# Kernel optimization log

Measured on AMD Instinct MI355X. Metric: run time of the kernel, lower is better.

Reference implementation:

```python
import jax, jax.numpy as jnp
import numpy as np

B, N, T_FULL, T, KS, FEAT = 32, 360, 512, 64, 8, 8
NLAYERS = 3   # DCGRU layers
GLAYERS = 4   # bidirectional GRU layers in GruKRegion


def _gru_layer(x, Wih, Whh, bih, bhh, reverse):
    # x: [M, Tg, in] -> [M, Tg, H]; PyTorch GRU gate order (r, z, n)
    M = x.shape[0]
    Hh = Whh.shape[1]
    xp = jnp.einsum('mti,gi->mtg', x, Wih) + bih  # precompute input projections
    if reverse:
        xp = xp[:, ::-1]

    def step(h, xg):
        gh = jnp.einsum('mh,gh->mg', h, Whh) + bhh
        xr, xz, xn = jnp.split(xg, 3, -1)
        hr, hz, hn = jnp.split(gh, 3, -1)
        r = jax.nn.sigmoid(xr + hr)
        z = jax.nn.sigmoid(xz + hz)
        n = jnp.tanh(xn + r * hn)
        hnew = (1.0 - z) * n + z * h
        return hnew, hnew

    _, hs = jax.lax.scan(step, jnp.zeros((M, Hh), x.dtype), jnp.swapaxes(xp, 0, 1))
    hs = jnp.swapaxes(hs, 0, 1)
    if reverse:
        hs = hs[:, ::-1]
    return hs


def _dcgru_cell(x, h, adj, gw, gb, cw, cb):
    # x, h: [B, N] (rnn_units = 1); adj: [B, N, N]; max_diffusion_step = 2
    def gconv(inp, st, W, bias):
        x0 = jnp.stack([inp, st], axis=-1)                     # [B,N,2]
        x1 = jnp.einsum('bnm,bmc->bnc', adj, x0)
        x2 = 2.0 * jnp.einsum('bnm,bmc->bnc', adj, x1) - x0    # Chebyshev recurrence
        # torch layout: [B,N,C,num_matrices] flattened channel-major
        xc = jnp.stack([x0, x1, x2], axis=-1).reshape(x0.shape[0], N, 6)
        return jnp.einsum('bnf,fo->bno', xc, W) + bias

    gates = jax.nn.sigmoid(gconv(x, h, gw, gb))                # [B,N,2]
    r, u = gates[..., 0], gates[..., 1]
    c = jnp.tanh(gconv(x, r * h, cw, cb)[..., 0])
    return u * h + (1.0 - u) * c


def _forward(full_seq, reconstruct_seq, node_feas, temperature,
             g0wih, g0whh, g0bih, g0bhh, gwih, gwhh, gbih, gbhh,
             l1w, l1b, l2w, l2b,
             enc_gw, enc_gb, enc_cw, enc_cb,
             dec_gw, dec_gb, dec_cw, dec_cb, proj_w, proj_b):
    b, n, tfull = full_seq.shape
    # ---- GruKRegion feature extractor ----
    x = full_seq.reshape(b * n, tfull // KS, KS)
    out = jnp.concatenate(
        [_gru_layer(x, g0wih[0], g0whh[0], g0bih[0], g0bhh[0], False),
         _gru_layer(x, g0wih[1], g0whh[1], g0bih[1], g0bhh[1], True)], axis=-1)
    for l in range(GLAYERS - 1):
        out = jnp.concatenate(
            [_gru_layer(out, gwih[l, 0], gwhh[l, 0], gbih[l, 0], gbhh[l, 0], False),
             _gru_layer(out, gwih[l, 1], gwhh[l, 1], gbih[l, 1], gbhh[l, 1], True)], axis=-1)
    feat = out[:, -1, :].reshape(b, n, 2 * KS)
    feat = jax.nn.leaky_relu(jnp.einsum('bnf,of->bno', feat, l1w) + l1b, 0.2)
    feat = jnp.einsum('bnf,of->bno', feat, l2w) + l2b          # [B,N,FEAT]
    # ---- Embed2GraphByProduct ----
    logits = jnp.einsum('bjk,bpk->bjp', feat, feat)            # [B,N,N]
    # ---- hard gumbel softmax ----
    U = jax.random.uniform(jax.random.key(42), logits.shape, logits.dtype)
    g = -jnp.log(-jnp.log(U + 1e-10) + 1e-10)
    y_soft = jax.nn.softmax((logits + g) / temperature, axis=-1)
    y_hard = jax.nn.one_hot(jnp.argmax(y_soft, -1), n, dtype=y_soft.dtype)
    adj = y_soft + jax.lax.stop_gradient(y_hard - y_soft)
    adj = jnp.where(jnp.eye(n, dtype=bool), 0.0, adj)          # zero diagonal
    # (original computes a random-walk matrix then discards it; skipped)
    # ---- encoder: scan over time, 3 stacked DCGRU layers ----
    seq = jnp.transpose(reconstruct_seq, (2, 0, 1))            # [T,B,N]

    def enc_step(hid, xt):
        o = xt
        new = []
        for l in range(NLAYERS):
            hnew = _dcgru_cell(o, hid[l], adj, enc_gw[l], enc_gb[l], enc_cw[l], enc_cb[l])
            new.append(hnew)
            o = hnew
        return jnp.stack(new), None

    hid, _ = jax.lax.scan(enc_step, jnp.zeros((NLAYERS, b, n), seq.dtype), seq)

    def dec_step(carry, _):
        hidc, inp = carry
        o = inp
        new = []
        for l in range(NLAYERS):
            hnew = _dcgru_cell(o, hidc[l], adj, dec_gw[l], dec_gb[l], dec_cw[l], dec_cb[l])
            new.append(hnew)
            o = hnew
        proj = o * proj_w[0, 0] + proj_b[0]                    # Linear(1,1)
        return (jnp.stack(new), proj), proj

    _, outs = jax.lax.scan(dec_step, (hid, jnp.zeros((b, n), seq.dtype)), None, length=T)
    return jnp.transpose(outs, (1, 2, 0))                      # [B,N,T]


def setup_inputs():
    key = jax.random.key(0)
    ks = jax.random.split(key, 24)
    s = 0.2
    p = lambda k, sh: jax.random.normal(k, sh, jnp.float32) * s
    return dict(
        full_seq=jax.random.normal(ks[0], (B, N, T_FULL), jnp.float32),
        reconstruct_seq=jax.random.normal(ks[1], (B, N, T), jnp.float32),
        node_feas=jax.random.normal(ks[2], (B, N, KS), jnp.float32),
        temperature=jnp.ones((), jnp.float32),
        g0wih=p(ks[3], (2, 3 * KS, KS)), g0whh=p(ks[4], (2, 3 * KS, KS)),
        g0bih=p(ks[5], (2, 3 * KS)), g0bhh=p(ks[6], (2, 3 * KS)),
        gwih=p(ks[7], (GLAYERS - 1, 2, 3 * KS, 2 * KS)),
        gwhh=p(ks[8], (GLAYERS - 1, 2, 3 * KS, KS)),
        gbih=p(ks[9], (GLAYERS - 1, 2, 3 * KS)), gbhh=p(ks[10], (GLAYERS - 1, 2, 3 * KS)),
        l1w=p(ks[11], (KS, 2 * KS)), l1b=p(ks[12], (KS,)),
        l2w=p(ks[13], (FEAT, KS)), l2b=p(ks[14], (FEAT,)),
        enc_gw=p(ks[15], (NLAYERS, 6, 2)), enc_gb=jnp.ones((NLAYERS, 2), jnp.float32),
        enc_cw=p(ks[16], (NLAYERS, 6, 1)), enc_cb=jnp.zeros((NLAYERS, 1), jnp.float32),
        dec_gw=p(ks[17], (NLAYERS, 6, 2)), dec_gb=jnp.ones((NLAYERS, 2), jnp.float32),
        dec_cw=p(ks[18], (NLAYERS, 6, 1)), dec_cb=jnp.zeros((NLAYERS, 1), jnp.float32),
        proj_w=p(ks[19], (1, 1)), proj_b=jnp.zeros((1,), jnp.float32),
    )


def reference(full_seq, reconstruct_seq, node_feas, temperature,
              g0wih, g0whh, g0bih, g0bhh, gwih, gwhh, gbih, gbhh,
              l1w, l1b, l2w, l2b,
              enc_gw, enc_gb, enc_cw, enc_cb,
              dec_gw, dec_gb, dec_cw, dec_cb, proj_w, proj_b):
    return _forward(full_seq, reconstruct_seq, node_feas, temperature,
                    g0wih, g0whh, g0bih, g0bhh, gwih, gwhh, gbih, gbhh,
                    l1w, l1b, l2w, l2b,
                    enc_gw, enc_gb, enc_cw, enc_cb,
                    dec_gw, dec_gb, dec_cw, dec_cb, proj_w, proj_b)
```

## Files before the change

kernel.cpp:

```cpp
#include <hip/hip_runtime.h>
#include <math.h>

#define M_SEQ 11520
#define NNODE 360
#define NB    32
#define TT    64

__device__ __forceinline__ float fsigd(float x)  { return 1.0f / (1.0f + __expf(-x)); }
__device__ __forceinline__ float ftanhd(float x) { return 1.0f - 2.0f / (__expf(2.0f * x) + 1.0f); }

__device__ __forceinline__ void lds_barrier()
{
    asm volatile("s_waitcnt lgkmcnt(0)" ::: "memory");
    __builtin_amdgcn_sched_barrier(0);
    __builtin_amdgcn_s_barrier();
    __builtin_amdgcn_sched_barrier(0);
}

__device__ __forceinline__ unsigned rotl32(unsigned x, int n) { return (x << n) | (x >> (32 - n)); }

__device__ __forceinline__ void tf2x32(unsigned& x0, unsigned& x1)
{
    const unsigned k0 = 0u, k1 = 42u, k2 = 0u ^ 42u ^ 0x1BD11BDAu;
    x0 += k0; x1 += k1;
#define R4(a,b,c,d) \
    x0 += x1; x1 = rotl32(x1,a); x1 ^= x0; \
    x0 += x1; x1 = rotl32(x1,b); x1 ^= x0; \
    x0 += x1; x1 = rotl32(x1,c); x1 ^= x0; \
    x0 += x1; x1 = rotl32(x1,d); x1 ^= x0;
    R4(13,15,26,6)   x0 += k1; x1 += k2 + 1u;
    R4(17,29,16,24)  x0 += k2; x1 += k0 + 2u;
    R4(13,15,26,6)   x0 += k0; x1 += k1 + 3u;
    R4(17,29,16,24)  x0 += k1; x1 += k2 + 4u;
    R4(13,15,26,6)   x0 += k2; x1 += k0 + 5u;
#undef R4
}

__device__ __forceinline__ float jax_uniform(unsigned idx)
{
    unsigned x0 = 0u, x1 = idx;
    tf2x32(x0, x1);
    unsigned bits = x0 ^ x1;
    return __uint_as_float((bits >> 9) | 0x3f800000u) - 1.0f;
}

template<int K>
__device__ __forceinline__ void swz_fma(float h, const float* w0, const float* w1,
                                        const float* w2, float& g0, float& g1, float& g2)
{
    float hk = __int_as_float(
        __builtin_amdgcn_ds_swizzle(__float_as_int(h), (K << 5) | 0x18));
    g0 += hk * w0[K];
    g1 += hk * w1[K];
    g2 += hk * w2[K];
    if constexpr (K < 7)
        swz_fma<K + 1>(h, w0, w1, w2, g0, g1, g2);
}

template<int I>
__device__ __forceinline__ void ldx(float* __restrict__ xv, const float* __restrict__ p)
{
    const float4* p4 = reinterpret_cast<const float4*>(p);
#pragma unroll
    for (int q = 0; q < I / 4; ++q) {
        float4 f = p4[q];
        xv[4*q] = f.x; xv[4*q+1] = f.y; xv[4*q+2] = f.z; xv[4*q+3] = f.w;
    }
}

template<int I>
__device__ __forceinline__ void xgates(const float* __restrict__ xv,
    const float* wx0, const float* wx1, const float* wx2,
    float bx0, float bx1, float bx2, float& xr, float& xz, float& xn)
{
    xr = bx0; xz = bx1; xn = bx2;
#pragma unroll
    for (int k = 0; k < I; ++k) {
        xr += xv[k] * wx0[k];
        xz += xv[k] * wx1[k];
        xn += xv[k] * wx2[k];
    }
}

__device__ __forceinline__ float hstep(float h, float xr, float xz, float xn,
    const float* w0, const float* w1, const float* w2,
    float bh0, float bh1, float bh2)
{
    float gh0 = bh0, gh1 = bh1, gh2 = bh2;
    swz_fma<0>(h, w0, w1, w2, gh0, gh1, gh2);
    float r  = fsigd(xr + gh0);
    float z  = fsigd(xz + gh1);
    float nn = ftanhd(xn + r * gh2);
    return (1.f - z) * nn + z * h;
}

template<int I, bool LASTONLY>
__global__ __launch_bounds__(256) void gru_fused(
    const float* __restrict__ x,
    const float* __restrict__ wih,
    const float* __restrict__ whh,
    const float* __restrict__ bih,
    const float* __restrict__ bhh,
    float* __restrict__ out)
{
    const int tid = blockIdx.x * 256 + threadIdx.x;
    const int j   = tid & 7;
    const int md  = tid >> 3;
    if (md >= M_SEQ * 2) return;
    const int m = md >> 1, dir = md & 1;

    float wx0[I], wx1[I], wx2[I];
    const float* WI = wih + dir * 24 * I;
#pragma unroll
    for (int k = 0; k < I; ++k) {
        wx0[k] = WI[j * I + k];
        wx1[k] = WI[(8 + j) * I + k];
        wx2[k] = WI[(16 + j) * I + k];
    }
    float w0[8], w1[8], w2[8];
    const float* WH = whh + dir * 192;
#pragma unroll
    for (int k = 0; k < 8; ++k) {
        w0[k] = WH[j * 8 + k];
        w1[k] = WH[(8 + j) * 8 + k];
        w2[k] = WH[(16 + j) * 8 + k];
    }
    const float bx0 = bih[dir*24 + j], bx1 = bih[dir*24 + 8 + j], bx2 = bih[dir*24 + 16 + j];
    const float bh0 = bhh[dir*24 + j], bh1 = bhh[dir*24 + 8 + j], bh2 = bhh[dir*24 + 16 + j];

    const float* xm = x + (size_t)m * TT * I;
    float* om = out + (size_t)m * TT * 16 + dir * 8 + j;

    const int tstep = dir ? -1 : 1;
    const int tbase = dir ? TT - 1 : 0;

    float h = 0.f;
    float xva[I], xvb[I];
    ldx<I>(xva, xm + (tbase) * I);
    ldx<I>(xvb, xm + (tbase + tstep) * I);
    float cr, cz, cn;
    xgates<I>(xva, wx0, wx1, wx2, bx0, bx1, bx2, cr, cz, cn);

    for (int tt = 0; tt < TT; tt += 2) {
        const int t0 = tbase + tstep * tt;
        const int t1 = t0 + tstep;
        if (tt + 2 < TT) ldx<I>(xva, xm + (t0 + 2 * tstep) * I);
        float nr, nz, nn;
        xgates<I>(xvb, wx0, wx1, wx2, bx0, bx1, bx2, nr, nz, nn);
        h = hstep(h, cr, cz, cn, w0, w1, w2, bh0, bh1, bh2);
        if (!LASTONLY || t0 == TT - 1) om[t0 * 16] = h;
        if (tt + 3 < TT) ldx<I>(xvb, xm + (t0 + 3 * tstep) * I);
        h = hstep(h, nr, nz, nn, w0, w1, w2, bh0, bh1, bh2);
        if (!LASTONLY || t1 == TT - 1) om[t1 * 16] = h;
        xgates<I>(xva, wx0, wx1, wx2, bx0, bx1, bx2, cr, cz, cn);
    }
}

__global__ void feat_kernel(const float* __restrict__ gout,
                            const float* __restrict__ l1w, const float* __restrict__ l1b,
                            const float* __restrict__ l2w, const float* __restrict__ l2b,
                            float* __restrict__ feat)
{
    int m = blockIdx.x * blockDim.x + threadIdx.x;
    if (m >= M_SEQ) return;
    const float* xp = gout + (size_t)m * TT * 16 + (TT - 1) * 16;
    float xv[16];
#pragma unroll
    for (int i = 0; i < 16; ++i) xv[i] = xp[i];
    float h1[8];
#pragma unroll
    for (int o = 0; o < 8; ++o) {
        float a = 0.f;
#pragma unroll
        for (int f = 0; f < 16; ++f) a += xv[f] * l1w[o * 16 + f];
        a += l1b[o];
        h1[o] = (a >= 0.f) ? a : 0.2f * a;
    }
#pragma unroll
    for (int o = 0; o < 8; ++o) {
        float a = 0.f;
#pragma unroll
        for (int f = 0; f < 8; ++f) a += h1[f] * l2w[o * 8 + f];
        feat[(size_t)m * 8 + o] = a + l2b[o];
    }
}

__global__ void adj_kernel(const float* __restrict__ feat,
                           const float* __restrict__ tptr,
                           int* __restrict__ colp, float* __restrict__ vp)
{
    const int gw   = (blockIdx.x * blockDim.x + threadIdx.x) >> 6;
    const int lane = threadIdx.x & 63;
    if (gw >= NB * NNODE) return;
    const int b = gw / NNODE;
    const int n = gw - b * NNODE;
    const float T = tptr[0];
    const float* fb = feat + (size_t)b * NNODE * 8;
    float fn[8];
#pragma unroll
    for (int k = 0; k < 8; ++k) fn[k] = fb[(size_t)n * 8 + k];

    float sv[6];
    float mval = -3.0e38f; int midx = 1 << 30;
#pragma unroll
    for (int s = 0; s < 6; ++s) {
        int p = s * 64 + lane;
        float xs = -3.0e38f;
        if (p < NNODE) {
            const float* fp = fb + (size_t)p * 8;
            float d = 0.f;
#pragma unroll
            for (int k = 0; k < 8; ++k) d += fn[k] * fp[k];
            unsigned idx = (unsigned)gw * 360u + (unsigned)p;
            float u   = jax_uniform(idx);
            float gum = -logf(-logf(u + 1e-10f) + 1e-10f);
            xs = (d + gum) / T;
            if (xs > mval) { mval = xs; midx = p; }
        }
        sv[s] = xs;
    }
    for (int off = 32; off > 0; off >>= 1) {
        float ov = __shfl_xor(mval, off);
        int   oi = __shfl_xor(midx, off);
        if (ov > mval || (ov == mval && oi < midx)) { mval = ov; midx = oi; }
    }
    float ssum = 0.f;
#pragma unroll
    for (int s = 0; s < 6; ++s) {
        int p = s * 64 + lane;
        if (p < NNODE) ssum += expf(sv[s] - mval);
    }
    for (int off = 32; off > 0; off >>= 1) ssum += __shfl_xor(ssum, off);
    if (lane == 0) {
        float ys = 1.0f / ssum;
        float v  = ys + (1.0f - ys);
        if (midx == n) v = 0.0f;
        colp[gw] = midx;
        vp[gw]   = v;
    }
}

__device__ __forceinline__ void dc_layer(
    bool comp,
    float o_own, float oa, float ob,
    float& hn, float ha, float hb,
    float v, float vv, int c1, int c2, bool act, int n,
    const float* __restrict__ W, float bgr, float bgu,
    const float* __restrict__ C, float cb,
    float* __restrict__ s_rh)
{
    float f1 = 0.f, f2 = 0.f, f4 = 0.f, f5 = 0.f, rh = 0.f;
    if (comp) {
        f1 = v * oa; f2 = vv * ob - o_own;
        f4 = v * ha; f5 = vv * hb - hn;
        float r = fsigd(o_own*W[0] + f1*W[2] + f2*W[4] + hn*W[6] + f4*W[8] + f5*W[10] + bgr);
        rh = r * hn;
        if (act) s_rh[n] = rh;
    }
    lds_barrier();
    if (comp) {
        float rha = s_rh[c1], rhb = s_rh[c2];
        float u  = fsigd(o_own*W[1] + f1*W[3] + f2*W[5] + hn*W[7] + f4*W[9] + f5*W[11] + bgu);
        float cnd = ftanhd(o_own*C[0] + f1*C[1] + f2*C[2] + rh*C[3]
                           + (v*rha)*C[4] + (vv*rhb - rh)*C[5] + cb);
        hn = u * hn + (1.f - u) * cnd;
    }
}

__global__ __launch_bounds__(768, 1) void decode_kernel(
    const float* __restrict__ rec,
    const int*   __restrict__ colp, const float* __restrict__ vp,
    const float* __restrict__ egw, const float* __restrict__ egb,
    const float* __restrict__ ecw, const float* __restrict__ ecb,
    const float* __restrict__ dgw, const float* __restrict__ dgb,
    const float* __restrict__ dcw, const float* __restrict__ dcb,
    const float* __restrict__ pw,  const float* __restrict__ pb,
    float* __restrict__ outp)
{
    __shared__ float s_h[2][3][NNODE];
    __shared__ float s_xe[2][NNODE];
    __shared__ float s_r1[2][NNODE];
    __shared__ float s_u1[2][NNODE];
    __shared__ float s_c1[2][NNODE];
    __shared__ float s_rh0[NNODE];
    __shared__ float s_rh2[NNODE];
    __shared__ float s_o[NNODE];
    __shared__ float s_rhd[NNODE];
    __shared__ float s_v[NNODE];
    __shared__ int   s_c[NNODE];

    const int  b    = blockIdx.x;
    const int  tid  = threadIdx.x;
    const bool isB  = tid >= 384;
    const bool isA  = !isB;
    const int  node = isB ? tid - 384 : tid;
    const bool actN = node < NNODE;

    const float* recb = rec + ((size_t)b * NNODE + node) * TT;

    float o_own = 0.f, xq1 = 0.f;
    if (isA && actN) {
        s_c[node] = colp[b * NNODE + node];
        s_v[node] = vp[b * NNODE + node];
        o_own = recb[0];
        xq1   = recb[1];
        s_xe[0][node] = o_own;
#pragma unroll
        for (int l = 0; l < 3; ++l) { s_h[0][l][node] = 0.f; s_h[1][l][node] = 0.f; }
    }
    __syncthreads();

    int c1 = 0, c2 = 0;
    float v = 0.f, vv = 0.f;
    if (actN) {
        c1 = s_c[node];
        c2 = s_c[c1];
        v  = s_v[node];
        vv = 2.f * v * s_v[c1];
    }
    const float projw = pw[0], projb = pb[0];

    float Wg[36], Bg[6], Wc[18], Cb[3];
#pragma unroll
    for (int k = 0; k < 36; ++k) Wg[k] = egw[k];
#pragma unroll
    for (int k = 0; k < 6;  ++k) Bg[k] = egb[k];
#pragma unroll
    for (int k = 0; k < 18; ++k) Wc[k] = ecw[k];
#pragma unroll
    for (int k = 0; k < 3;  ++k) Cb[k] = ecb[k];

    float h0r = 0.f, h1r = 0.f, h2r = 0.f;

    for (int k = 0; k <= TT; ++k) {
        const int  pk = k & 1, qk = pk ^ 1;
        const bool aAct = isA && actN && (k < TT);
        const bool bAct = isB && actN && (k >= 1);
        float nx2 = 0.f;
        if (aAct && k + 2 < TT) nx2 = recb[k + 2];

        float fA1=0.f, fA2=0.f, fA4=0.f, fA5=0.f, rhA=0.f;
        if (isA) {
            float xa  = s_xe[pk][c1],   xb  = s_xe[pk][c2];
            float h0a = s_h[pk][0][c1], h0b = s_h[pk][0][c2];
            fA1 = v * xa;  fA2 = vv * xb - o_own;
            fA4 = v * h0a; fA5 = vv * h0b - h0r;
            float rA = fsigd(o_own*Wg[0] + fA1*Wg[2] + fA2*Wg[4] + h0r*Wg[6]
                             + fA4*Wg[8] + fA5*Wg[10] + Bg[0]);
            rhA = rA * h0r;
            if (aAct) s_rh0[node] = rhA;
        } else {
            float rh1o = s_r1[pk][node];
            float rh1a = s_r1[pk][c1], rh1b = s_r1[pk][c2];
            float u1v  = s_u1[pk][node], cp1v = s_c1[pk][node];
            float cnd1 = ftanhd(cp1v + rh1o*Wc[9] + (v*rh1a)*Wc[10]
                                + (vv*rh1b - rh1o)*Wc[11] + Cb[1]);
            if (bAct) { h1r = u1v * h1r + (1.f - u1v) * cnd1; s_h[qk][1][node] = h1r; }
        }
        lds_barrier();

        float fB1=0.f, fB2=0.f, fB4=0.f, fB5=0.f, rhB=0.f;
        if (isA) {
            float rh0a = s_rh0[c1], rh0b = s_rh0[c2];
            float uA = fsigd(o_own*Wg[1] + fA1*Wg[3] + fA2*Wg[5] + h0r*Wg[7]
                             + fA4*Wg[9] + fA5*Wg[11] + Bg[1]);
            float cndA = ftanhd(o_own*Wc[0] + fA1*Wc[1] + fA2*Wc[2] + rhA*Wc[3]
                                + (v*rh0a)*Wc[4] + (vv*rh0b - rhA)*Wc[5] + Cb[0]);
            if (aAct) {
                h0r = uA * h0r + (1.f - uA) * cndA;
                s_h[qk][0][node] = h0r;
                s_xe[qk][node]   = xq1;
            }
        } else {
            float o2a = s_h[qk][1][c1], o2b = s_h[qk][1][c2];
            float h2a = s_h[pk][2][c1], h2b = s_h[pk][2][c2];
            fB1 = v * o2a; fB2 = vv * o2b - h1r;
            fB4 = v * h2a; fB5 = vv * h2b - h2r;
            float rB = fsigd(h1r*Wg[24] + fB1*Wg[26] + fB2*Wg[28] + h2r*Wg[30]
                             + fB4*Wg[32] + fB5*Wg[34] + Bg[4]);
            rhB = rB * h2r;
            if (bAct) s_rh2[node] = rhB;
        }
        lds_barrier();

        if (isA) {
            float o1a = s_h[qk][0][c1], o1b = s_h[qk][0][c2];
            float h1own = s_h[qk][1][node];
            float h1a = s_h[qk][1][c1], h1b = s_h[qk][1][c2];
            float fC1 = v * o1a, fC2 = vv * o1b - h0r;
            float fC4 = v * h1a, fC5 = vv * h1b - h1own;
            float r1 = fsigd(h0r*Wg[12] + fC1*Wg[14] + fC2*Wg[16] + h1own*Wg[18]
                             + fC4*Wg[20] + fC5*Wg[22] + Bg[2]);
            float u1 = fsigd(h0r*Wg[13] + fC1*Wg[15] + fC2*Wg[17] + h1own*Wg[19]
                             + fC4*Wg[21] + fC5*Wg[23] + Bg[3]);
            float cp1 = h0r*Wc[6] + fC1*Wc[7] + fC2*Wc[8];
            if (aAct) { s_r1[qk][node] = r1 * h1own; s_u1[qk][node] = u1; s_c1[qk][node] = cp1; }
        } else {
            float rh2a = s_rh2[c1], rh2b = s_rh2[c2];
            float u2 = fsigd(h1r*Wg[25] + fB1*Wg[27] + fB2*Wg[29] + h2r*Wg[31]
                             + fB4*Wg[33] + fB5*Wg[35] + Bg[5]);
            float cnd2 = ftanhd(h1r*Wc[12] + fB1*Wc[13] + fB2*Wc[14] + rhB*Wc[15]
                                + (v*rh2a)*Wc[16] + (vv*rh2b - rhB)*Wc[17] + Cb[2]);
            if (bAct) { h2r = u2 * h2r + (1.f - u2) * cnd2; s_h[qk][2][node] = h2r; }
        }
        lds_barrier();
        if (isA) { o_own = xq1; xq1 = nx2; }
    }

    if (tid < NNODE) {
        s_h[0][1][tid] = s_h[1][1][tid];
        s_h[0][2][tid] = s_h[1][2][tid];
        s_xe[0][tid]   = 0.f;
    }
    __syncthreads();

    const bool actd = (isA && actN);
    const int  nd   = actN ? node : 0;
    float hreg[3];
    hreg[0] = h0r;
    hreg[1] = s_h[0][1][nd];
    hreg[2] = s_h[0][2][nd];

#pragma unroll
    for (int k = 0; k < 36; ++k) Wg[k] = dgw[k];
#pragma unroll
    for (int k = 0; k < 6;  ++k) Bg[k] = dgb[k];
#pragma unroll
    for (int k = 0; k < 18; ++k) Wc[k] = dcw[k];
#pragma unroll
    for (int k = 0; k < 3;  ++k) Cb[k] = dcb[k];

    float dinp = 0.f;
    int p = 0;
    for (int t = 0; t < TT; ++t) {
        float xa=0.f, xb=0.f;
        float h0a=0.f,h0b=0.f,h1a=0.f,h1b=0.f,h2a=0.f,h2b=0.f;
        if (isA) {
            xa  = s_xe[p][c1];     xb  = s_xe[p][c2];
            h0a = s_h[p][0][c1];   h0b = s_h[p][0][c2];
            h1a = s_h[p][1][c1];   h1b = s_h[p][1][c2];
            h2a = s_h[p][2][c1];   h2b = s_h[p][2][c2];
        }
        const int q = p ^ 1;
        dc_layer(isA, dinp, xa, xb, hreg[0], h0a, h0b, v, vv, c1, c2, actd, node,
                 Wg, Bg[0], Bg[1], Wc, Cb[0], s_rhd);
        if (actd) { s_h[q][0][node] = hreg[0]; s_o[node] = hreg[0]; }
        lds_barrier();
        float oa=0.f, ob=0.f;
        if (isA) { oa = s_o[c1]; ob = s_o[c2]; }
        dc_layer(isA, hreg[0], oa, ob, hreg[1], h1a, h1b, v, vv, c1, c2, actd, node,
                 Wg + 12, Bg[2], Bg[3], Wc + 6, Cb[1], s_rhd);
        if (actd) { s_h[q][1][node] = hreg[1]; s_o[node] = hreg[1]; }
        lds_barrier();
        if (isA) { oa = s_o[c1]; ob = s_o[c2]; }
        dc_layer(isA, hreg[1], oa, ob, hreg[2], h2a, h2b, v, vv, c1, c2, actd, node,
                 Wg + 24, Bg[4], Bg[5], Wc + 12, Cb[2], s_rhd);
        float proj = hreg[2] * projw + projb;
        if (actd) {
            s_h[q][2][node] = hreg[2];
            s_xe[q][node]   = proj;
            outp[((size_t)b * NNODE + node) * TT + t] = proj;
        }
        lds_barrier();
        dinp = proj; p = q;
    }
}

extern "C" void kernel_launch(void* const* d_in, const int* in_sizes, int n_in,
                              void* d_out, int out_size, void* d_ws, size_t ws_size,
                              hipStream_t stream)
{
    (void)in_sizes; (void)n_in; (void)out_size; (void)ws_size;
    const float* full_seq = (const float*)d_in[0];
    const float* rec_seq  = (const float*)d_in[1];
    const float* temp     = (const float*)d_in[3];
    const float* g0wih    = (const float*)d_in[4];
    const float* g0whh    = (const float*)d_in[5];
    const float* g0bih    = (const float*)d_in[6];
    const float* g0bhh    = (const float*)d_in[7];
    const float* gwih     = (const float*)d_in[8];
    const float* gwhh     = (const float*)d_in[9];
    const float* gbih     = (const float*)d_in[10];
    const float* gbhh     = (const float*)d_in[11];
    const float* l1w      = (const float*)d_in[12];
    const float* l1b      = (const float*)d_in[13];
    const float* l2w      = (const float*)d_in[14];
    const float* l2b      = (const float*)d_in[15];
    const float* enc_gw   = (const float*)d_in[16];
    const float* enc_gb   = (const float*)d_in[17];
    const float* enc_cw   = (const float*)d_in[18];
    const float* enc_cb   = (const float*)d_in[19];
    const float* dec_gw   = (const float*)d_in[20];
    const float* dec_gb   = (const float*)d_in[21];
    const float* dec_cw   = (const float*)d_in[22];
    const float* dec_cb   = (const float*)d_in[23];
    const float* proj_w   = (const float*)d_in[24];
    const float* proj_b   = (const float*)d_in[25];
    float* outp = (float*)d_out;

    float* ws   = (float*)d_ws;
    float* feat = ws;
    float* vbuf = feat + (size_t)M_SEQ * 8;
    int*   cbuf = (int*)(vbuf + M_SEQ);
    float* bufA = (float*)(cbuf + M_SEQ);
    float* bufB = bufA + (size_t)M_SEQ * TT * 16;

    const int ggru = (M_SEQ * 2 * 8) / 256;
    gru_fused<8,false><<<ggru, 256, 0, stream>>>(full_seq, g0wih, g0whh, g0bih, g0bhh, bufA);
    gru_fused<16,false><<<ggru, 256, 0, stream>>>(bufA, gwih + 0 * 768, gwhh + 0 * 384,
                                                  gbih + 0 * 48, gbhh + 0 * 48, bufB);
    gru_fused<16,false><<<ggru, 256, 0, stream>>>(bufB, gwih + 1 * 768, gwhh + 1 * 384,
                                                  gbih + 1 * 48, gbhh + 1 * 48, bufA);
    gru_fused<16,true><<<ggru, 256, 0, stream>>>(bufA, gwih + 2 * 768, gwhh + 2 * 384,
                                                 gbih + 2 * 48, gbhh + 2 * 48, bufB);
    feat_kernel<<<M_SEQ / 256, 256, 0, stream>>>(bufB, l1w, l1b, l2w, l2b, feat);
    adj_kernel<<<(NB * NNODE) / 4, 256, 0, stream>>>(feat, temp, cbuf, vbuf);
    decode_kernel<<<NB, 768, 0, stream>>>(rec_seq, cbuf, vbuf,
                                          enc_gw, enc_gb, enc_cw, enc_cb,
                                          dec_gw, dec_gb, dec_cw, dec_cb,
                                          proj_w, proj_b, outp);
}
```

Measured before the change: 512.7 us.

## Fuse four GRU layers into one kernel with LDS intermediate buffers

New measurement: 674.0 us. 31.5% more time.

```diff
diff --git a/kernel.cpp b/kernel.cpp
--- a/kernel.cpp
+++ b/kernel.cpp
@@ -94,21 +94,14 @@
     return (1.f - z) * nn + z * h;
 }
 
-template<int I, bool LASTONLY>
-__global__ __launch_bounds__(256) void gru_fused(
-    const float* __restrict__ x,
-    const float* __restrict__ wih,
-    const float* __restrict__ whh,
-    const float* __restrict__ bih,
-    const float* __restrict__ bhh,
-    float* __restrict__ out)
-{
-    const int tid = blockIdx.x * 256 + threadIdx.x;
-    const int j   = tid & 7;
-    const int md  = tid >> 3;
-    if (md >= M_SEQ * 2) return;
-    const int m = md >> 1, dir = md & 1;
-
+template<int I, bool GIN, bool LAST>
+__device__ __forceinline__ void gru_layer(
+    const float* __restrict__ xin,
+    float* __restrict__ outw,
+    const float* __restrict__ wih, const float* __restrict__ whh,
+    const float* __restrict__ bih, const float* __restrict__ bhh,
+    int j, int dir, int mloc)
+{
     float wx0[I], wx1[I], wx2[I];
     const float* WI = wih + dir * 24 * I;
 #pragma unroll
@@ -128,32 +121,67 @@
     const float bx0 = bih[dir*24 + j], bx1 = bih[dir*24 + 8 + j], bx2 = bih[dir*24 + 16 + j];
     const float bh0 = bhh[dir*24 + j], bh1 = bhh[dir*24 + 8 + j], bh2 = bhh[dir*24 + 16 + j];
 
-    const float* xm = x + (size_t)m * TT * I;
-    float* om = out + (size_t)m * TT * 16 + dir * 8 + j;
-
     const int tstep = dir ? -1 : 1;
     const int tbase = dir ? TT - 1 : 0;
 
+#define XADDR(t) (GIN ? (xin + (t) * I) : (xin + (t) * 64 + mloc * 16))
+
     float h = 0.f;
     float xva[I], xvb[I];
-    ldx<I>(xva, xm + (tbase) * I);
-    ldx<I>(xvb, xm + (tbase + tstep) * I);
+    ldx<I>(xva, XADDR(tbase));
+    ldx<I>(xvb, XADDR(tbase + tstep));
     float cr, cz, cn;
     xgates<I>(xva, wx0, wx1, wx2, bx0, bx1, bx2, cr, cz, cn);
 
     for (int tt = 0; tt < TT; tt += 2) {
         const int t0 = tbase + tstep * tt;
         const int t1 = t0 + tstep;
-        if (tt + 2 < TT) ldx<I>(xva, xm + (t0 + 2 * tstep) * I);
+        if (tt + 2 < TT) ldx<I>(xva, XADDR(t0 + 2 * tstep));
         float nr, nz, nn;
         xgates<I>(xvb, wx0, wx1, wx2, bx0, bx1, bx2, nr, nz, nn);
         h = hstep(h, cr, cz, cn, w0, w1, w2, bh0, bh1, bh2);
-        if (!LASTONLY || t0 == TT - 1) om[t0 * 16] = h;
-        if (tt + 3 < TT) ldx<I>(xvb, xm + (t0 + 3 * tstep) * I);
+        if constexpr (LAST) { if (t0 == TT - 1) outw[t0 * 16] = h; }
+        else                outw[t0 * 64 + mloc * 16 + dir * 8 + j] = h;
+        if (tt + 3 < TT) ldx<I>(xvb, XADDR(t0 + 3 * tstep));
         h = hstep(h, nr, nz, nn, w0, w1, w2, bh0, bh1, bh2);
-        if (!LASTONLY || t1 == TT - 1) om[t1 * 16] = h;
+        if constexpr (LAST) { if (t1 == TT - 1) outw[t1 * 16] = h; }
+        else                outw[t1 * 64 + mloc * 16 + dir * 8 + j] = h;
         xgates<I>(xva, wx0, wx1, wx2, bx0, bx1, bx2, cr, cz, cn);
     }
+#undef XADDR
+}
+
+__global__ __launch_bounds__(64) void gru4_fused(
+    const float* __restrict__ x0,
+    const float* __restrict__ g0wih, const float* __restrict__ g0whh,
+    const float* __restrict__ g0bih, const float* __restrict__ g0bhh,
+    const float* __restrict__ gwih,  const float* __restrict__ gwhh,
+    const float* __restrict__ gbih,  const float* __restrict__ gbhh,
+    float* __restrict__ out)
+{
+    __shared__ float bufA[TT * 64];
+    __shared__ float bufB[TT * 64];
+
+    const int lane = threadIdx.x;
+    const int j    = lane & 7;
+    const int dir  = (lane >> 3) & 1;
+    const int mloc = lane >> 4;
+    const int m    = blockIdx.x * 4 + mloc;
+
+    gru_layer<8, true, false>(x0 + (size_t)m * TT * 8, bufA,
+                              g0wih, g0whh, g0bih, g0bhh, j, dir, mloc);
+    __syncthreads();
+    gru_layer<16, false, false>(bufA, bufB,
+                                gwih + 0 * 768, gwhh + 0 * 384,
+                                gbih + 0 * 48,  gbhh + 0 * 48, j, dir, mloc);
+    __syncthreads();
+    gru_layer<16, false, false>(bufB, bufA,
+                                gwih + 1 * 768, gwhh + 1 * 384,
+                                gbih + 1 * 48,  gbhh + 1 * 48, j, dir, mloc);
+    __syncthreads();
+    gru_layer<16, false, true>(bufA, out + (size_t)m * TT * 16 + dir * 8 + j,
+                               gwih + 2 * 768, gwhh + 2 * 384,
+                               gbih + 2 * 48,  gbhh + 2 * 48, j, dir, mloc);
 }
 
 __global__ void feat_kernel(const float* __restrict__ gout,
@@ -504,15 +532,11 @@
     int*   cbuf = (int*)(vbuf + M_SEQ);
     float* bufA = (float*)(cbuf + M_SEQ);
     float* bufB = bufA + (size_t)M_SEQ * TT * 16;
-
-    const int ggru = (M_SEQ * 2 * 8) / 256;
-    gru_fused<8,false><<<ggru, 256, 0, stream>>>(full_seq, g0wih, g0whh, g0bih, g0bhh, bufA);
-    gru_fused<16,false><<<ggru, 256, 0, stream>>>(bufA, gwih + 0 * 768, gwhh + 0 * 384,
-                                                  gbih + 0 * 48, gbhh + 0 * 48, bufB);
-    gru_fused<16,false><<<ggru, 256, 0, stream>>>(bufB, gwih + 1 * 768, gwhh + 1 * 384,
-                                                  gbih + 1 * 48, gbhh + 1 * 48, bufA);
-    gru_fused<16,true><<<ggru, 256, 0, stream>>>(bufA, gwih + 2 * 768, gwhh + 2 * 384,
-                                                 gbih + 2 * 48, gbhh + 2 * 48, bufB);
+    (void)bufA;
+
+    gru4_fused<<<M_SEQ / 4, 64, 0, stream>>>(full_seq,
+                                             g0wih, g0whh, g0bih, g0bhh,
+                                             gwih, gwhh, gbih, gbhh, bufB);
     feat_kernel<<<M_SEQ / 256, 256, 0, stream>>>(bufB, l1w, l1b, l2w, l2b, feat);
     adj_kernel<<<(NB * NNODE) / 4, 256, 0, stream>>>(feat, temp, cbuf, vbuf);
     decode_kernel<<<NB, 768, 0, stream>>>(rec_seq, cbuf, vbuf,
```
